# Kernel optimization log

Hardware: AMD Instinct MI355X
Metric: run time of the kernel (lower is better)

The kernel has to match this reference:

```python
import jax, jax.numpy as jnp
import numpy as np

IN_F = 4096
OUT_F = 4096
GROUP = 128          # group_size
N_GROUPS = IN_F // GROUP  # 32
PACK = 8             # 32-bit word / 4-bit values


def setup_inputs() -> dict:
    key = jax.random.key(0)
    k1, k2, k3, k4, k5 = jax.random.split(key, 5)
    x = jax.random.normal(k1, (4, 2048, IN_F), dtype=jnp.float32)
    # packed int4 weights: each int32 holds 8 nibbles along the in_features dim
    q_weights = jax.random.randint(
        k2, (IN_F // PACK, OUT_F),
        jnp.iinfo(jnp.int32).min, jnp.iinfo(jnp.int32).max, dtype=jnp.int32)
    scales = jax.random.uniform(k3, (N_GROUPS, OUT_F), jnp.float32, 0.005, 0.02)
    # zeros stored in absolute (scale-premultiplied) units, GPTQ-style
    zeros = jax.random.uniform(k4, (N_GROUPS, OUT_F), jnp.float32, 0.0, 0.16)
    bias = jax.random.normal(k5, (OUT_F,), dtype=jnp.float32) * 0.01
    return {"x": x, "q_weights": q_weights, "scales": scales,
            "zeros": zeros, "bias": bias}


def _dequantize(q_weights, scales, zeros):
    # Unpack 8 nibbles per int32 word along in_features.
    shifts = (jnp.arange(PACK, dtype=jnp.int32) * 4)
    nib = (q_weights[:, None, :] >> shifts[None, :, None]) & 0xF  # (P, 8, O)
    q = nib.reshape(IN_F, OUT_F).astype(jnp.float32)              # (I, O)
    s = jnp.repeat(scales, GROUP, axis=0)                         # (I, O)
    z = jnp.repeat(zeros, GROUP, axis=0)                          # (I, O)
    return q * s - z


def reference(x, q_weights, scales, zeros, bias):
    # W[i, o] = scale[g(i), o] * q[i, o] - zero[g(i), o];  y = x @ W + bias
    W = _dequantize(q_weights, scales, zeros)
    out = jnp.einsum('bsi,io->bso', x, W)
    return out + bias[None, None, :]
```

## Files before the change

### kernel.cpp

```cpp
#include <hip/hip_runtime.h>
#include <hip/hip_bf16.h>

#define K_DIM 4096
#define N_DIM 4096
#define M_DIM 8192

typedef __bf16 bf16x8 __attribute__((ext_vector_type(8)));
typedef float floatx4 __attribute__((ext_vector_type(4)));

__device__ __forceinline__ unsigned short f2bf(float f) {
    union { float f; unsigned u; } v; v.f = f;
    unsigned u = v.u;
    return (unsigned short)((u + 0x7FFFu + ((u >> 16) & 1u)) >> 16);
}

__global__ __launch_bounds__(256) void cast_x_kernel(const float* __restrict__ x,
                                                     unsigned short* __restrict__ xb) {
    const int t = blockIdx.x * 256 + threadIdx.x;
    const int base = t * 8;
    float4 f0 = *(const float4*)(x + base);
    float4 f1 = *(const float4*)(x + base + 4);
    int4 o;
    o.x = (int)f2bf(f0.x) | ((int)f2bf(f0.y) << 16);
    o.y = (int)f2bf(f0.z) | ((int)f2bf(f0.w) << 16);
    o.z = (int)f2bf(f1.x) | ((int)f2bf(f1.y) << 16);
    o.w = (int)f2bf(f1.z) | ((int)f2bf(f1.w) << 16);
    *(int4*)(xb + base) = o;
}

__global__ __launch_bounds__(256) void dequant_kernel(const int* __restrict__ qw,
                                                      const float* __restrict__ scales,
                                                      const float* __restrict__ zeros,
                                                      unsigned short* __restrict__ wt) {
    __shared__ int4 lds[128 * 8];
    const int tid = threadIdx.x;
    const int nb = (blockIdx.x & 31) * 128;
    const int kb = blockIdx.x >> 5;
    const int p0 = kb * 8;
    const int g = kb >> 1;

#pragma unroll
    for (int it = 0; it < 4; ++it) {
        const int w = tid + it * 256;
        const int p = w >> 7;
        const int n = w & 127;
        const unsigned word = (unsigned)qw[(p0 + p) * N_DIM + nb + n];
        const float s = scales[g * N_DIM + nb + n];
        const float z = zeros[g * N_DIM + nb + n];
        unsigned short h[8];
#pragma unroll
        for (int j = 0; j < 8; ++j) {
            float q = (float)((word >> (4 * j)) & 0xFu);
            h[j] = f2bf(q * s - z);
        }
        int4 o;
        o.x = (int)h[0] | ((int)h[1] << 16);
        o.y = (int)h[2] | ((int)h[3] << 16);
        o.z = (int)h[4] | ((int)h[5] << 16);
        o.w = (int)h[6] | ((int)h[7] << 16);
        lds[n * 8 + (p ^ (n & 7))] = o;
    }
    __syncthreads();

#pragma unroll
    for (int it = 0; it < 4; ++it) {
        const int r = (tid >> 3) + it * 32;
        const int oc = tid & 7;
        int4 v = lds[r * 8 + (oc ^ (r & 7))];
        *(int4*)(wt + (size_t)(nb + r) * K_DIM + kb * 64 + oc * 8) = v;
    }
}

__global__ __launch_bounds__(256) void gemm_kernel(const unsigned short* __restrict__ A,
                                                   const unsigned short* __restrict__ B,
                                                   const float* __restrict__ bias,
                                                   float* __restrict__ C) {
    __shared__ unsigned short As[128 * 64];
    __shared__ unsigned short Bs[128 * 64];

    const int tid = threadIdx.x;
    const int lane = tid & 63;
    const int wave = tid >> 6;
    const int tileM = blockIdx.y * 128;
    const int tileN = blockIdx.x * 128;

    const int srow = tid >> 3;
    const int scol = ((tid & 7) ^ (srow & 7)) * 8;
    const int aBase = (tileM + srow) * K_DIM + scol;
    const int bBase = (tileN + srow) * K_DIM + scol;
    const int ldsOff = tid * 8;

    floatx4 acc[4][4];
#pragma unroll
    for (int i = 0; i < 4; ++i)
#pragma unroll
        for (int j = 0; j < 4; ++j) acc[i][j] = (floatx4){0.f, 0.f, 0.f, 0.f};

    const int m0 = (wave >> 1) * 64;
    const int n0 = (wave & 1) * 64;
    const int frow = lane & 15;
    const int fkq = lane >> 4;
    const int sw = lane & 7;

    for (int k0 = 0; k0 < K_DIM; k0 += 64) {
#pragma unroll
        for (int j = 0; j < 4; ++j) {
            __builtin_amdgcn_global_load_lds(
                (__attribute__((address_space(1))) void*)(A + aBase + k0 + j * 32 * K_DIM),
                (__attribute__((address_space(3))) void*)(&As[j * 2048 + ldsOff]),
                16, 0, 0);
            __builtin_amdgcn_global_load_lds(
                (__attribute__((address_space(1))) void*)(B + bBase + k0 + j * 32 * K_DIM),
                (__attribute__((address_space(3))) void*)(&Bs[j * 2048 + ldsOff]),
                16, 0, 0);
        }
        __syncthreads();

#pragma unroll
        for (int kk = 0; kk < 64; kk += 32) {
            const int jc = (kk >> 3) + fkq;
            const int ch = (jc ^ sw) << 3;
            bf16x8 a[4], b[4];
#pragma unroll
            for (int i = 0; i < 4; ++i)
                a[i] = *(const bf16x8*)&As[(m0 + i * 16 + frow) * 64 + ch];
#pragma unroll
            for (int i = 0; i < 4; ++i)
                b[i] = *(const bf16x8*)&Bs[(n0 + i * 16 + frow) * 64 + ch];
#pragma unroll
            for (int mi = 0; mi < 4; ++mi)
#pragma unroll
                for (int ni = 0; ni < 4; ++ni)
                    acc[mi][ni] = __builtin_amdgcn_mfma_f32_16x16x32_bf16(
                        a[mi], b[ni], acc[mi][ni], 0, 0, 0);
        }
        __syncthreads();
    }

    const int crow = (lane >> 4) * 4;
    const int ccol = lane & 15;
#pragma unroll
    for (int ni = 0; ni < 4; ++ni) {
        const int gcol = tileN + n0 + ni * 16 + ccol;
        const float bv = bias[gcol];
#pragma unroll
        for (int mi = 0; mi < 4; ++mi) {
            const int rbase = (tileM + m0 + mi * 16 + crow) * N_DIM + gcol;
#pragma unroll
            for (int r = 0; r < 4; ++r)
                C[rbase + r * N_DIM] = acc[mi][ni][r] + bv;
        }
    }
}

extern "C" void kernel_launch(void* const* d_in, const int* in_sizes, int n_in,
                              void* d_out, int out_size, void* d_ws, size_t ws_size,
                              hipStream_t stream) {
    (void)in_sizes; (void)n_in; (void)out_size; (void)ws_size;
    const float* x      = (const float*)d_in[0];
    const int*   qw     = (const int*)d_in[1];
    const float* scales = (const float*)d_in[2];
    const float* zeros  = (const float*)d_in[3];
    const float* bias   = (const float*)d_in[4];
    float* out = (float*)d_out;

    unsigned short* xb = (unsigned short*)d_ws;
    unsigned short* wt = xb + (size_t)M_DIM * K_DIM;

    hipLaunchKernelGGL(cast_x_kernel, dim3(16384), dim3(256), 0, stream, x, xb);
    hipLaunchKernelGGL(dequant_kernel, dim3(2048), dim3(256), 0, stream, qw, scales, zeros, wt);
    hipLaunchKernelGGL(gemm_kernel, dim3(32, 64), dim3(256), 0, stream, xb, wt, bias, out);
}
```

Measured before the change: 493.8 us.

## Rewrite GEMM as 256x256 8-wave double-buffered pipelined MFMA kernel

Replaces the 128x128, 4-wave, single-buffer GEMM with a 256x256 tile computed by 512 threads. Each wave owns a 128x64 sub-tile and accumulates it in four quarters. Global-to-LDS loads for the next K-steps are double-buffered and interleaved between MFMA phases, with explicit waitcnt, barriers and setprio, so memory traffic overlaps compute. A block-index swizzle is added for L2 locality. The aim is higher arithmetic intensity and better MFMA utilisation. In exchange it uses 128KB of LDS and many accumulator registers, which limits occupancy, and the hand-tuned barrier and waitcnt sequencing is fragile.

```diff
diff --git a/kernel.cpp b/kernel.cpp
--- a/kernel.cpp
+++ b/kernel.cpp
@@ -4,6 +4,7 @@
 #define K_DIM 4096
 #define N_DIM 4096
 #define M_DIM 8192
+#define NT 64
 
 typedef __bf16 bf16x8 __attribute__((ext_vector_type(8)));
 typedef float floatx4 __attribute__((ext_vector_type(4)));
@@ -71,71 +72,162 @@
     }
 }
 
-__global__ __launch_bounds__(256) void gemm_kernel(const unsigned short* __restrict__ A,
-                                                   const unsigned short* __restrict__ B,
-                                                   const float* __restrict__ bias,
-                                                   float* __restrict__ C) {
-    __shared__ unsigned short As[128 * 64];
-    __shared__ unsigned short Bs[128 * 64];
+__device__ __forceinline__ void gl_lds16(const unsigned short* g, unsigned short* l) {
+    __builtin_amdgcn_global_load_lds((__attribute__((address_space(1))) void*)g,
+                                     (__attribute__((address_space(3))) void*)l, 16, 0, 0);
+}
+
+__global__ __launch_bounds__(512, 2) void gemm_kernel(const unsigned short* __restrict__ A,
+                                                      const unsigned short* __restrict__ B,
+                                                      const float* __restrict__ bias,
+                                                      float* __restrict__ C) {
+    __shared__ unsigned short As[2 * 256 * 64];
+    __shared__ unsigned short Bs[2 * 256 * 64];
 
     const int tid = threadIdx.x;
     const int lane = tid & 63;
     const int wave = tid >> 6;
-    const int tileM = blockIdx.y * 128;
-    const int tileN = blockIdx.x * 128;
-
-    const int srow = tid >> 3;
-    const int scol = ((tid & 7) ^ (srow & 7)) * 8;
-    const int aBase = (tileM + srow) * K_DIM + scol;
-    const int bBase = (tileN + srow) * K_DIM + scol;
-    const int ldsOff = tid * 8;
-
-    floatx4 acc[4][4];
-#pragma unroll
-    for (int i = 0; i < 4; ++i)
-#pragma unroll
-        for (int j = 0; j < 4; ++j) acc[i][j] = (floatx4){0.f, 0.f, 0.f, 0.f};
-
-    const int m0 = (wave >> 1) * 64;
-    const int n0 = (wave & 1) * 64;
+
+    int bid = blockIdx.x;
+    bid = (bid & 7) * 64 + (bid >> 3);
+    const int tileM = (bid >> 4) * 256;
+    const int tileN = (bid & 15) * 256;
+
+    const int m0 = (wave >> 2) * 128;
+    const int n0 = (wave & 3) * 64;
     const int frow = lane & 15;
     const int fkq = lane >> 4;
-    const int sw = lane & 7;
-
-    for (int k0 = 0; k0 < K_DIM; k0 += 64) {
-#pragma unroll
-        for (int j = 0; j < 4; ++j) {
-            __builtin_amdgcn_global_load_lds(
-                (__attribute__((address_space(1))) void*)(A + aBase + k0 + j * 32 * K_DIM),
-                (__attribute__((address_space(3))) void*)(&As[j * 2048 + ldsOff]),
-                16, 0, 0);
-            __builtin_amdgcn_global_load_lds(
-                (__attribute__((address_space(1))) void*)(B + bBase + k0 + j * 32 * K_DIM),
-                (__attribute__((address_space(3))) void*)(&Bs[j * 2048 + ldsOff]),
-                16, 0, 0);
-        }
-        __syncthreads();
-
-#pragma unroll
-        for (int kk = 0; kk < 64; kk += 32) {
-            const int jc = (kk >> 3) + fkq;
-            const int ch = (jc ^ sw) << 3;
-            bf16x8 a[4], b[4];
-#pragma unroll
-            for (int i = 0; i < 4; ++i)
-                a[i] = *(const bf16x8*)&As[(m0 + i * 16 + frow) * 64 + ch];
-#pragma unroll
-            for (int i = 0; i < 4; ++i)
-                b[i] = *(const bf16x8*)&Bs[(n0 + i * 16 + frow) * 64 + ch];
-#pragma unroll
-            for (int mi = 0; mi < 4; ++mi)
-#pragma unroll
-                for (int ni = 0; ni < 4; ++ni)
+    const int sw = frow & 7;
+    const int ch0 = (fkq ^ sw) << 3;
+    const int ch1 = ((fkq ^ sw) ^ 4) << 3;
+
+    const int r0 = tid >> 3;
+    const int kcg = (tid & 7) ^ (r0 & 7);
+    const int dst0 = tid * 8;
+
+    const unsigned short* Abase = A + (size_t)(tileM + r0) * K_DIM + kcg * 8;
+    const unsigned short* Bbase = B + (size_t)(tileN + r0) * K_DIM + kcg * 8;
+
+#define STAGE_A(T, H, BUF) do {                                                        \
+        const unsigned short* _s = Abase + (size_t)(H) * (128 * K_DIM) + (T) * 64;     \
+        gl_lds16(_s, &As[((BUF) << 14) + ((H) << 13) + dst0]);                         \
+        gl_lds16(_s + 64 * K_DIM, &As[((BUF) << 14) + ((H) << 13) + 4096 + dst0]);     \
+    } while (0)
+#define STAGE_B(T, H, BUF) do {                                                        \
+        const unsigned short* _s = Bbase + (size_t)(H) * (128 * K_DIM) + (T) * 64;     \
+        gl_lds16(_s, &Bs[((BUF) << 14) + ((H) << 13) + dst0]);                         \
+        gl_lds16(_s + 64 * K_DIM, &Bs[((BUF) << 14) + ((H) << 13) + 4096 + dst0]);     \
+    } while (0)
+
+    floatx4 acc[8][4];
+#pragma unroll
+    for (int i = 0; i < 8; ++i)
+#pragma unroll
+        for (int j = 0; j < 4; ++j) acc[i][j] = (floatx4){0.f, 0.f, 0.f, 0.f};
+
+    STAGE_B(0, 0, 0); STAGE_B(0, 1, 0); STAGE_A(0, 0, 0); STAGE_A(0, 1, 0);
+    STAGE_B(1, 0, 1); STAGE_B(1, 1, 1); STAGE_A(1, 0, 1);
+    asm volatile("s_waitcnt vmcnt(6)" ::: "memory");
+    __builtin_amdgcn_s_barrier();
+
+    bf16x8 a[4][2], b[4][2];
+
+#pragma unroll 2
+    for (int t = 0; t < NT; ++t) {
+        const int buf = t & 1;
+        const int bo = buf << 14;
+
+#pragma unroll
+        for (int mi = 0; mi < 4; ++mi) {
+            const int row = m0 + mi * 16 + frow;
+            a[mi][0] = *(const bf16x8*)&As[bo + row * 64 + ch0];
+            a[mi][1] = *(const bf16x8*)&As[bo + row * 64 + ch1];
+        }
+#pragma unroll
+        for (int ni = 0; ni < 4; ++ni) {
+            const int row = n0 + ni * 16 + frow;
+            b[ni][0] = *(const bf16x8*)&Bs[bo + row * 64 + ch0];
+            b[ni][1] = *(const bf16x8*)&Bs[bo + row * 64 + ch1];
+        }
+        if (t + 1 < NT) STAGE_A(t + 1, 1, buf ^ 1);
+        asm volatile("s_waitcnt lgkmcnt(8)" ::: "memory");
+        __builtin_amdgcn_s_barrier();
+        asm volatile("s_waitcnt lgkmcnt(0)" ::: "memory");
+        __builtin_amdgcn_sched_barrier(0);
+        __builtin_amdgcn_s_setprio(1);
+#pragma unroll
+        for (int mi = 0; mi < 4; ++mi)
+#pragma unroll
+            for (int ni = 0; ni < 2; ++ni)
+#pragma unroll
+                for (int kh = 0; kh < 2; ++kh)
                     acc[mi][ni] = __builtin_amdgcn_mfma_f32_16x16x32_bf16(
-                        a[mi], b[ni], acc[mi][ni], 0, 0, 0);
-        }
-        __syncthreads();
-    }
+                        a[mi][kh], b[ni][kh], acc[mi][ni], 0, 0, 0);
+        __builtin_amdgcn_s_setprio(0);
+        __builtin_amdgcn_sched_barrier(0);
+        __builtin_amdgcn_s_barrier();
+
+        if (t + 2 < NT) STAGE_B(t + 2, 0, buf);
+        __builtin_amdgcn_s_barrier();
+        __builtin_amdgcn_sched_barrier(0);
+        __builtin_amdgcn_s_setprio(1);
+#pragma unroll
+        for (int mi = 0; mi < 4; ++mi)
+#pragma unroll
+            for (int ni = 2; ni < 4; ++ni)
+#pragma unroll
+                for (int kh = 0; kh < 2; ++kh)
+                    acc[mi][ni] = __builtin_amdgcn_mfma_f32_16x16x32_bf16(
+                        a[mi][kh], b[ni][kh], acc[mi][ni], 0, 0, 0);
+        __builtin_amdgcn_s_setprio(0);
+        __builtin_amdgcn_sched_barrier(0);
+        __builtin_amdgcn_s_barrier();
+
+#pragma unroll
+        for (int mi = 0; mi < 4; ++mi) {
+            const int row = m0 + 64 + mi * 16 + frow;
+            a[mi][0] = *(const bf16x8*)&As[bo + row * 64 + ch0];
+            a[mi][1] = *(const bf16x8*)&As[bo + row * 64 + ch1];
+        }
+        if (t + 2 < NT) STAGE_B(t + 2, 1, buf);
+        __builtin_amdgcn_s_barrier();
+        asm volatile("s_waitcnt lgkmcnt(0)" ::: "memory");
+        __builtin_amdgcn_sched_barrier(0);
+        __builtin_amdgcn_s_setprio(1);
+#pragma unroll
+        for (int mi = 0; mi < 4; ++mi)
+#pragma unroll
+            for (int ni = 2; ni < 4; ++ni)
+#pragma unroll
+                for (int kh = 0; kh < 2; ++kh)
+                    acc[4 + mi][ni] = __builtin_amdgcn_mfma_f32_16x16x32_bf16(
+                        a[mi][kh], b[ni][kh], acc[4 + mi][ni], 0, 0, 0);
+        __builtin_amdgcn_s_setprio(0);
+        __builtin_amdgcn_sched_barrier(0);
+        __builtin_amdgcn_s_barrier();
+
+        if (t + 2 < NT) STAGE_A(t + 2, 0, buf);
+        __builtin_amdgcn_s_barrier();
+        __builtin_amdgcn_sched_barrier(0);
+        __builtin_amdgcn_s_setprio(1);
+#pragma unroll
+        for (int mi = 0; mi < 4; ++mi)
+#pragma unroll
+            for (int ni = 0; ni < 2; ++ni)
+#pragma unroll
+                for (int kh = 0; kh < 2; ++kh)
+                    acc[4 + mi][ni] = __builtin_amdgcn_mfma_f32_16x16x32_bf16(
+                        a[mi][kh], b[ni][kh], acc[4 + mi][ni], 0, 0, 0);
+        __builtin_amdgcn_s_setprio(0);
+        if (t + 2 < NT) { asm volatile("s_waitcnt vmcnt(6)" ::: "memory"); }
+        else            { asm volatile("s_waitcnt vmcnt(0)" ::: "memory"); }
+        __builtin_amdgcn_sched_barrier(0);
+        __builtin_amdgcn_s_barrier();
+    }
+#undef STAGE_A
+#undef STAGE_B
+
+    asm volatile("s_waitcnt vmcnt(0)" ::: "memory");
 
     const int crow = (lane >> 4) * 4;
     const int ccol = lane & 15;
@@ -144,7 +236,7 @@
         const int gcol = tileN + n0 + ni * 16 + ccol;
         const float bv = bias[gcol];
 #pragma unroll
-        for (int mi = 0; mi < 4; ++mi) {
+        for (int mi = 0; mi < 8; ++mi) {
             const int rbase = (tileM + m0 + mi * 16 + crow) * N_DIM + gcol;
 #pragma unroll
             for (int r = 0; r < 4; ++r)
@@ -169,5 +261,5 @@
 
     hipLaunchKernelGGL(cast_x_kernel, dim3(16384), dim3(256), 0, stream, x, xb);
     hipLaunchKernelGGL(dequant_kernel, dim3(2048), dim3(256), 0, stream, qw, scales, zeros, wt);
-    hipLaunchKernelGGL(gemm_kernel, dim3(32, 64), dim3(256), 0, stream, xb, wt, bias, out);
-}
+    hipLaunchKernelGGL(gemm_kernel, dim3(512), dim3(512), 0, stream, xb, wt, bias, out);
+}
```

Measured after the change: 470.4 us. 1.05x faster.
